# Kernel optimization log

Measured on AMD Instinct MI355X. Metric: run time of the kernel, lower is better.

The kernel has to match this reference:

```python
import math
import jax, jax.numpy as jnp
import numpy as np

B, N, W, D, H = 16, 64, 128, 128, 4

def posenc(L, d):
    pos = jnp.arange(L, dtype=jnp.float32)[:, None]
    div = jnp.exp(jnp.arange(0, d, 2, dtype=jnp.float32) * (-math.log(10000.0) / d))
    pe = jnp.zeros((L, d), jnp.float32)
    pe = pe.at[:, 0::2].set(jnp.sin(pos * div))
    pe = pe.at[:, 1::2].set(jnp.cos(pos * div))
    return pe

def ln(x):
    # torch nn.LayerNorm(x.shape[1:]) created fresh each call: normalize over all non-batch dims, no affine
    ax = tuple(range(1, x.ndim))
    m = x.mean(ax, keepdims=True)
    v = ((x - m) ** 2).mean(ax, keepdims=True)
    return (x - m) / jnp.sqrt(v + 1e-5)

def conv1d(x, w, b):
    # x [B,C,L], w [Cout,Cin,K] (torch layout), VALID padding
    y = jax.lax.conv_general_dilated(x, w, (1,), 'VALID', dimension_numbers=('NCH', 'OIH', 'NCH'))
    return y + b[None, :, None]

def convt1d(x, w, b, stride, pad):
    # torch ConvTranspose1d, w [Cin,Cout,K]
    K = w.shape[2]
    w_ = jnp.flip(w, 2).transpose(1, 0, 2)  # [Cout,Cin,K]
    y = jax.lax.conv_general_dilated(x, w_, (1,), [(K - 1 - pad, K - 1 - pad)],
                                     lhs_dilation=(stride,), dimension_numbers=('NCH', 'OIH', 'NCH'))
    return y + b[None, :, None]

def mha(q, k, v, wi, bi, wo, bo):
    # torch nn.MultiheadAttention(batch_first=True), H heads
    d = q.shape[-1]
    qp = q @ wi[:d].T + bi[:d]
    kp = k @ wi[d:2 * d].T + bi[d:2 * d]
    vp = v @ wi[2 * d:].T + bi[2 * d:]
    def heads(t):
        b_, l_, _ = t.shape
        return t.reshape(b_, l_, H, d // H).transpose(0, 2, 1, 3)
    qh, kh, vh = heads(qp), heads(kp), heads(vp)
    s = jnp.einsum('bhqd,bhkd->bhqk', qh, kh) / jnp.sqrt(jnp.asarray(d // H, qh.dtype))
    o = jnp.einsum('bhqk,bhkd->bhqd', jax.nn.softmax(s, -1), vh)
    b_, l_ = q.shape[0], q.shape[1]
    return o.transpose(0, 2, 1, 3).reshape(b_, l_, d) @ wo.T + bo


def setup_inputs():
    key = jax.random.key(0)
    ks = iter(jax.random.split(key, 64))
    def w(shape, s=0.05):
        return jax.random.normal(next(ks), shape, jnp.float32) * s
    inp = {}
    inp['tokens'] = jax.random.randint(next(ks), (B, N, W), 0, 257, jnp.int32)
    inp['emb_table'] = w((257, D), 1.0)
    for nm in ['ce', 'ct', 'cg', 'ces', 'cts']:
        inp['w_' + nm] = w((D, D, 3))
        inp['b_' + nm] = w((D,))
    inp['mha_wi'] = w((3 * D, D)); inp['mha_bi'] = w((3 * D,))
    inp['mha_wo'] = w((D, D)); inp['mha_bo'] = w((D,))
    s = 1.0 / math.sqrt(D)
    inp['tgt1'] = jax.random.uniform(next(ks), (1, D), jnp.float32, -s, s)
    inp['tgt2'] = jax.random.uniform(next(ks), (1, D), jnp.float32, -s, s)
    for nm in ['mu', 'lv', 'di']:
        inp['w_' + nm] = w((D, D)); inp['b_' + nm] = w((D,))
    inp['eps'] = jax.random.normal(next(ks), (B, D), jnp.float32)
    inp['dk_w'] = w((32, 32)); inp['dk_b'] = w((32,))
    inp['dv_w'] = w((32, 32)); inp['dv_b'] = w((32,))
    inp['wt1'] = w((32, 64, 3)); inp['bt1'] = w((64,))
    inp['wt2'] = w((64, 128, 3)); inp['bt2'] = w((128,))
    for nm in ['sq', 'sk', 'sv']:
        inp[nm + '_w'] = w((128, 128)); inp[nm + '_b'] = w((128,))
    inp['wt3'] = w((128, 128, 3)); inp['bt3'] = w((128,))
    return inp


def reference(tokens, emb_table, w_ce, b_ce, w_ct, b_ct, w_cg, b_cg, w_ces, b_ces, w_cts, b_cts,
              mha_wi, mha_bi, mha_wo, mha_bo, tgt1, tgt2,
              w_mu, b_mu, w_lv, b_lv, w_di, b_di, eps,
              dk_w, dk_b, dv_w, dv_b, wt1, bt1, wt2, bt2,
              sq_w, sq_b, sk_w, sk_b, sv_w, sv_b, wt3, bt3):
    emb = emb_table[tokens] + posenc(W, D)                    # [B,N,W,D]
    flat = emb.reshape(B * N, W, D)                           # batch the per-sample torch loop

    def word_branch(wc, bc, act):
        h = act(conv1d(flat.transpose(0, 2, 1), wc, bc)).transpose(0, 2, 1)  # [BN,W-2,D]
        return mha(h, h, h, mha_wi, mha_bi, mha_wo, mha_bo)

    a_e = jax.nn.elu(word_branch(w_ce, b_ce, jax.nn.elu))
    a_t = jnp.tanh(word_branch(w_ct, b_ct, jnp.tanh))
    xw = ln((a_e * a_t).reshape(B, N, W - 2, D)).reshape(B * N, W - 2, D)

    h = jax.nn.elu(conv1d(xw.transpose(0, 2, 1), w_cg, b_cg)).transpose(0, 2, 1)  # [BN,W-4,D]
    q1 = jnp.broadcast_to(tgt1[None], (B * N, 1, D))
    out = mha(q1, h, h, mha_wi, mha_bi, mha_wo, mha_bo)[:, 0, :].reshape(B, N, D)

    se = out + posenc(N, D)                                   # sentence level

    def sent_branch(wc, bc, act):
        hh = act(conv1d(se.transpose(0, 2, 1), wc, bc)).transpose(0, 2, 1)       # [B,N-2,D]
        return mha(hh, hh, hh, mha_wi, mha_bi, mha_wo, mha_bo)

    s_e = jax.nn.elu(sent_branch(w_ces, b_ces, jax.nn.elu))
    s_t = jnp.tanh(sent_branch(w_cts, b_cts, jnp.tanh))
    xs = ln(s_e * s_t)
    q2 = jnp.broadcast_to(tgt2[None], (B, 1, D))
    doc = mha(q2, xs, xs, mha_wi, mha_bi, mha_wo, mha_bo)[:, 0, :]

    mu = doc @ w_mu.T + b_mu
    lv = doc @ w_lv.T + b_lv
    z = mu + eps * jnp.exp(0.5 * lv)

    h = (z @ w_di.T + b_di).reshape(B, 32, -1)                # [B,32,4]
    L = h.shape[2]
    k = jnp.einsum('oi,bil->bol', dk_w, h) + dk_b[None, :, None]
    v = jnp.einsum('oi,bil->bol', dv_w, h) + dv_b[None, :, None]
    kh = k.reshape(B, H, 8, L)
    vh = v.reshape(B, H, 8, L)
    att = jax.nn.softmax(jnp.einsum('bhdl,bhdm->bhlm', kh, vh) / jnp.sqrt(8.0), -1)
    h = jax.nn.elu(jnp.einsum('bhlm,bhdm->bhld', att, vh).reshape(B, 32, L))
    h = jax.nn.elu(ln(convt1d(h, wt1, bt1, 2, 1)))            # [B,64,7]
    h = jax.nn.elu(ln(convt1d(h, wt2, bt2, 2, 1)))            # [B,128,13]
    L2 = h.shape[2]
    qc = jnp.einsum('oi,bil->bol', sq_w, h) + sq_b[None, :, None]
    kc = jnp.einsum('oi,bil->bol', sk_w, h) + sk_b[None, :, None]
    vc = jnp.einsum('oi,bil->bol', sv_w, h) + sv_b[None, :, None]
    qh = qc.reshape(B, H, 32, L2)
    khh = kc.reshape(B, H, 32, L2)
    att = jax.nn.softmax(jnp.einsum('bhdl,bhdm->bhlm', qh, khh) / jnp.sqrt(32.0), -1)
    vr = vc.reshape(B, H, 32, L2).reshape(B, H, L2, 32)       # faithful torch .view reinterpretation
    h = jax.nn.elu(jnp.einsum('bhlm,bhmd->bhld', att, vr).reshape(B, 128, L2))
    recon = jax.nn.sigmoid(ln(convt1d(h, wt3, bt3, 1, 1)))    # [B,128,13]
    return recon, mu, lv
```

## Files before the change

kernel.cpp:

```cpp
#include <hip/hip_runtime.h>
#include <hip/hip_bf16.h>

typedef __hip_bfloat16 bf16;
typedef __attribute__((ext_vector_type(8))) short bf16x8;
typedef __attribute__((ext_vector_type(4))) float f32x4;

__device__ __forceinline__ float b2f(bf16 x){ return __bfloat162float(x); }
__device__ __forceinline__ bf16  f2b(float x){ return __float2bfloat16(x); }
__device__ __forceinline__ unsigned short b2u(bf16 x){ union{bf16 b; unsigned short u;} c; c.b = x; return c.u; }

#define LOG2E 1.4426950408889634f
#define QSC (0.17677669529663687f * LOG2E)

__device__ __forceinline__ float fexp2(float x){
  float r; asm("v_exp_f32 %0, %1" : "=v"(r) : "v"(x)); return r;
}
__device__ __forceinline__ float fast_exp(float x){ return fexp2(x * LOG2E); }
__device__ __forceinline__ float eluf(float x){ return x > 0.f ? x : fast_exp(x) - 1.f; }
__device__ __forceinline__ float fast_tanh(float x){
  float cx = fminf(fmaxf(x, -15.f), 15.f);
  float t = fexp2(cx * (2.f*LOG2E));
  return (t - 1.f) / (t + 1.f);
}

#define PE_C (-0.07195578415606394f)

__device__ __forceinline__ float pe_val(int pos, int d){
  int j2 = d & ~1;
  float ang = (float)pos * expf((float)j2 * PE_C);
  return (d & 1) ? cosf(ang) : sinf(ang);
}

__device__ __forceinline__ void pack_one(const float* __restrict__ W, bf16* __restrict__ out,
                                         int K, int N, int conv, int qscale, int t){
  int j = t & 7, lane = (t >> 3) & 63;
  int rest = t >> 9; int NT = N >> 4;
  int nt = rest % NT; int kb = rest / NT;
  int k = kb*32 + ((lane >> 4) << 3) + j;
  int n = nt*16 + (lane & 15);
  float v = conv ? W[n*384 + (k & 127)*3 + (k >> 7)] : W[(long)n*K + k];
  if (qscale && n < 128) v *= QSC;
  out[t] = f2b(v);
}

__global__ void k_prep(const float* __restrict__ w_ce, const float* __restrict__ w_ct,
                       const float* __restrict__ w_cg, const float* __restrict__ w_ces,
                       const float* __restrict__ w_cts, const float* __restrict__ wi,
                       const float* __restrict__ wo,
                       bf16* P_CE, bf16* P_CT, bf16* P_CG, bf16* P_CES, bf16* P_CTS,
                       bf16* P_WI, bf16* P_WO, float* __restrict__ pet){
  int bid = blockIdx.x;
  if (bid < 1152){
    int grp = bid / 192; int t = (bid % 192)*256 + threadIdx.x;
    const float* W; bf16* out; int K, N, conv, qs = 0;
    if      (grp == 0){ W = w_ce;  out = P_CE;  K=384; N=128; conv=1; }
    else if (grp == 1){ W = w_ct;  out = P_CT;  K=384; N=128; conv=1; }
    else if (grp == 2){ W = w_cg;  out = P_CG;  K=384; N=128; conv=1; }
    else if (grp == 3){ W = w_ces; out = P_CES; K=384; N=128; conv=1; }
    else if (grp == 4){ W = w_cts; out = P_CTS; K=384; N=128; conv=1; }
    else              { W = wi;    out = P_WI;  K=128; N=384; conv=0; qs=1; }
    pack_one(W, out, K, N, conv, qs, t);
  } else if (bid < 1216){
    int t = (bid - 1152)*256 + threadIdx.x;
    pack_one(wo, P_WO, 128, 128, 0, 0, t);
  } else {
    int i = (bid - 1216)*256 + threadIdx.x;
    if (i < 16384) pet[i] = pe_val(i >> 7, i & 127);
  }
}

__global__ void k_qprep(const float* __restrict__ wi, const float* __restrict__ bi,
                        const float* __restrict__ t1, const float* __restrict__ t2,
                        float* __restrict__ rkv){
  int tid = threadIdx.x;
  __shared__ float qps[256];
  {
    int which = tid >> 7, jj = tid & 127;
    const float* t = which ? t2 : t1;
    float a = bi[jj];
    for (int i = 0; i < 128; ++i) a += wi[jj*128 + i] * t[i];
    qps[tid] = a;
  }
  __syncthreads();
  int i = tid & 127, which = tid >> 7;
  for (int h = 0; h < 4; ++h){
    float a = 0.f;
    for (int d = 0; d < 32; ++d) a += qps[which*128 + h*32 + d] * wi[(128 + h*32 + d)*128 + i];
    rkv[which*512 + h*128 + i] = a;
  }
}

__global__ void k_embed8(const int* __restrict__ tok, const float* __restrict__ tab,
                         const float* __restrict__ pet, bf16* __restrict__ out){
  int t = blockIdx.x*256 + threadIdx.x;
  int q = t & 15;
  int flat = t >> 4; int w = flat & 127;
  int tk = tok[flat];
  const float* ta = tab + tk*128 + q*8;
  const float* pe = pet + (w << 7) + q*8;
  bf16 ob[8];
  #pragma unroll
  for (int i = 0; i < 8; ++i) ob[i] = f2b(ta[i] + pe[i]);
  *(f32x4*)(out + (size_t)t*8) = *(f32x4*)ob;
}

__global__ void k_se(const bf16* __restrict__ in, const float* __restrict__ pet, bf16* __restrict__ out){
  int idx = blockIdx.x*256 + threadIdx.x;
  int d = idx & 127; int n = (idx >> 7) & 63;
  out[idx] = f2b(b2f(in[idx]) + pet[(n << 7) + d]);
}

__global__ __launch_bounds__(256)
void k_gemm_mfma(const bf16* __restrict__ A, const bf16* __restrict__ Bp_, const bf16* __restrict__ Bp2,
                 const float* __restrict__ bias_, const float* __restrict__ bias2,
                 bf16* __restrict__ C_, bf16* __restrict__ C2p,
                 const bf16* __restrict__ mul,
                 int M, int K, int a_lout, int a_lind, int lda,
                 int NT, int n0t, int ldc, int act_, int act2,
                 const float* __restrict__ lnst, int lngrp){
  const bf16* Bp = Bp_; const float* bias = bias_; bf16* C = C_; int act = act_;
  if (blockIdx.z){ Bp = Bp2; bias = bias2; C = C2p; act = act2; }

  __shared__ f32x4 AsV[2][512];
  char* As0 = (char*)AsV[0];
  char* As1 = (char*)AsV[1];
  int tid = threadIdx.x;
  int lane = tid & 63, wave = tid >> 6;
  int wm = wave >> 1, wn = wave & 1;
  int m0 = blockIdx.x*128;
  int by = blockIdx.y;

  long offA[2]; bool okA[2]; float lnm[2], lnr[2]; int sbyte[2];
  #pragma unroll
  for (int p = 0; p < 2; ++p){
    int e = tid + p*256;
    int row = e >> 2, kq = e & 3, m = m0 + row;
    okA[p] = (m < M);
    long off = 0;
    if (okA[p]){
      off = (a_lout > 0) ? (long)(m / a_lout)*a_lind + (long)(m % a_lout)*128 + kq*8
                         : (long)m*lda + kq*8;
    }
    offA[p] = off;
    lnm[p] = 0.f; lnr[p] = 1.f;
    if (lnst && okA[p]){ int g = (int)(off / (long)lngrp); lnm[p] = lnst[2*g]; lnr[p] = lnst[2*g+1]; }
    sbyte[p] = (row*64 + kq*16) ^ ((row & 7) << 4);
  }
  auto loadA = [&](int p, int kb)->float4{
    float4 v = make_float4(0.f,0.f,0.f,0.f);
    if (okA[p]){
      v = *(const float4*)(A + offA[p] + kb*32);
      if (lnst){
        bf16* pp = (bf16*)&v; bf16 oo[8];
        #pragma unroll
        for (int u = 0; u < 8; ++u) oo[u] = f2b((b2f(pp[u]) - lnm[p]) * lnr[p]);
        v = *(float4*)&oo[0];
      }
    }
    return v;
  };

  const bf16* bptr[4];
  size_t bstep = (size_t)NT*512;
  #pragma unroll
  for (int fn = 0; fn < 4; ++fn){
    int ntile = n0t + by*8 + wn*4 + fn;
    bptr[fn] = Bp + ((size_t)ntile*64 + lane)*8;
  }
  int abyte[4];
  #pragma unroll
  for (int fm = 0; fm < 4; ++fm){
    int row = wm*64 + fm*16 + (lane & 15);
    abyte[fm] = (row*64 + ((lane >> 4) << 4)) ^ ((row & 7) << 4);
  }

  f32x4 acc[4][4];
  #pragma unroll
  for (int i = 0; i < 4; ++i)
    #pragma unroll
    for (int j = 0; j < 4; ++j) acc[i][j] = (f32x4){0.f,0.f,0.f,0.f};

  float4 va0 = loadA(0, 0), va1 = loadA(1, 0);
  *(float4*)(As0 + sbyte[0]) = va0;
  *(float4*)(As0 + sbyte[1]) = va1;
  __syncthreads();

  int nk = K >> 5;
  for (int kb = 0; kb < nk; ++kb){
    char* cur = (kb & 1) ? As1 : As0;
    char* nxt = (kb & 1) ? As0 : As1;
    bool more = (kb + 1) < nk;
    if (more){ va0 = loadA(0, kb+1); va1 = loadA(1, kb+1); }
    bf16x8 bfr[4];
    #pragma unroll
    for (int fn = 0; fn < 4; ++fn) bfr[fn] = *(const bf16x8*)(bptr[fn] + (size_t)kb*bstep);
    bf16x8 afr[4];
    #pragma unroll
    for (int fm = 0; fm < 4; ++fm) afr[fm] = *(const bf16x8*)(cur + abyte[fm]);
    #pragma unroll
    for (int fm = 0; fm < 4; ++fm)
      #pragma unroll
      for (int fn = 0; fn < 4; ++fn)
        acc[fm][fn] = __builtin_amdgcn_mfma_f32_16x16x32_bf16(afr[fm], bfr[fn], acc[fm][fn], 0, 0, 0);
    if (more){
      *(float4*)(nxt + sbyte[0]) = va0;
      *(float4*)(nxt + sbyte[1]) = va1;
    }
    __syncthreads();
  }

  #pragma unroll
  for (int fm = 0; fm < 4; ++fm){
    #pragma unroll
    for (int r = 0; r < 4; ++r){
      int m = m0 + wm*64 + fm*16 + ((lane >> 4) << 2) + r;
      if (m >= M) continue;
      #pragma unroll
      for (int fn = 0; fn < 4; ++fn){
        int n = by*128 + wn*64 + fn*16 + (lane & 15);
        float v = acc[fm][fn][r] + (bias ? bias[n] : 0.f);
        if (act == 1) v = eluf(v);
        else if (act == 2) v = fast_tanh(v);
        if (mul) v *= b2f(mul[(long)m*ldc + n]);
        C[(long)m*ldc + n] = f2b(v);
      }
    }
  }
}

template<int L>
__global__ __launch_bounds__(256)
void k_attn_fused(const bf16* __restrict__ X, const bf16* __restrict__ Pwi,
                  const float* __restrict__ bi, bf16* __restrict__ o){
  constexpr int KB  = (L + 31) / 32;
  constexpr int MT  = KB * 2;
  constexpr int WMT = MT / 4;
  constexpr int NP  = KB * 32;
  constexpr int PRS = NP * 2;

  __shared__ alignas(16) char As[NP*256];
  __shared__ alignas(16) char Qb[NP*64];
  __shared__ alignas(16) char Kb[NP*64];
  __shared__ alignas(16) char Vt[32*PRS];
  char* Pb = As;

  int tid = threadIdx.x;
  int s = blockIdx.x >> 2, h = blockIdx.x & 3;
  const bf16* xb = X + (size_t)s*L*128;

  for (int e = tid; e < NP*16; e += 256){
    int row = e >> 4, c = e & 15;
    float4 v = make_float4(0.f,0.f,0.f,0.f);
    if (row < L) v = *(const float4*)(xb + (size_t)row*128 + c*8);
    *(float4*)(As + ((row*256 + c*16) ^ ((row & 7) << 4))) = v;
  }
  __syncthreads();

  int lane = tid & 63, wave = tid >> 6;
  int col = lane & 15;

  __builtin_amdgcn_s_setprio(1);
  #pragma unroll
  for (int mt = 0; mt < WMT; ++mt){
    int mtile = wave*WMT + mt;
    int arow = mtile*16 + col;
    bf16x8 a4[4];
    #pragma unroll
    for (int kb = 0; kb < 4; ++kb)
      a4[kb] = *(const bf16x8*)(As + ((arow*256 + kb*64 + ((lane >> 4) << 4)) ^ ((arow & 7) << 4)));
    #pragma unroll
    for (int which = 0; which < 3; ++which){
      f32x4 av[2];
      #pragma unroll
      for (int nt = 0; nt < 2; ++nt){
        int ntile = which*8 + h*2 + nt;
        float bia = bi[which*128 + h*32 + nt*16 + col];
        if (which == 0) bia *= QSC;
        av[nt] = (f32x4){bia, bia, bia, bia};
        #pragma unroll
        for (int kb = 0; kb < 4; ++kb){
          bf16x8 bfr = *(const bf16x8*)(Pwi + (((size_t)kb*24 + ntile)*64 + lane)*8);
          av[nt] = __builtin_amdgcn_mfma_f32_16x16x32_bf16(a4[kb], bfr, av[nt], 0, 0, 0);
        }
      }
      #pragma unroll
      for (int r = 0; r < 4; ++r){
        int row = mtile*16 + ((lane >> 4) << 2) + r;
        if (which < 2){
          unsigned pk = (unsigned)b2u(f2b(av[0][r])) | ((unsigned)b2u(f2b(av[1][r])) << 16);
          char* dst = which ? Kb : Qb;
          *(unsigned*)(dst + ((row*64 + col*4) ^ ((row & 7) << 4))) = pk;
        } else {
          int pos = (row & 15)*MT + (row >> 4);
          #pragma unroll
          for (int nt = 0; nt < 2; ++nt){
            int d = nt*16 + col;
            *(bf16*)(Vt + ((d*PRS + pos*2) ^ ((d & 7) << 4))) = f2b(av[nt][r]);
          }
        }
      }
    }
  }
  __builtin_amdgcn_s_setprio(0);
  __syncthreads();

  f32x4 acc[WMT][MT];
  #pragma unroll
  for (int mt = 0; mt < WMT; ++mt)
    #pragma unroll
    for (int nt = 0; nt < MT; ++nt) acc[mt][nt] = (f32x4){0.f,0.f,0.f,0.f};

  bf16x8 af[WMT];
  #pragma unroll
  for (int mt = 0; mt < WMT; ++mt){
    int row = (wave*WMT + mt)*16 + col;
    af[mt] = *(const bf16x8*)(Qb + ((row*64 + ((lane >> 4) << 4)) ^ ((row & 7) << 4)));
  }
  __builtin_amdgcn_s_setprio(1);
  #pragma unroll
  for (int nt = 0; nt < MT; ++nt){
    int rk2 = nt*16 + col;
    bf16x8 bfk = *(const bf16x8*)(Kb + ((rk2*64 + ((lane >> 4) << 4)) ^ ((rk2 & 7) << 4)));
    #pragma unroll
    for (int mt = 0; mt < WMT; ++mt)
      acc[mt][nt] = __builtin_amdgcn_mfma_f32_16x16x32_bf16(af[mt], bfk, acc[mt][nt], 0, 0, 0);
  }
  __builtin_amdgcn_s_setprio(0);

  const bool lastMask = col >= (L - (MT-1)*16);
  float pinv[WMT][4];
  #pragma unroll
  for (int mt = 0; mt < WMT; ++mt){
    #pragma unroll
    for (int r = 0; r < 4; ++r){
      float mx = -1e30f;
      #pragma unroll
      for (int nt = 0; nt < MT; ++nt){
        float v = acc[mt][nt][r];
        if (nt == MT-1 && lastMask){ v = -1e30f; acc[mt][nt][r] = v; }
        mx = fmaxf(mx, v);
      }
      mx = fmaxf(mx, __shfl_xor(mx, 1));
      mx = fmaxf(mx, __shfl_xor(mx, 2));
      mx = fmaxf(mx, __shfl_xor(mx, 4));
      mx = fmaxf(mx, __shfl_xor(mx, 8));
      float sum = 0.f;
      bf16 prow[MT];
      #pragma unroll
      for (int nt = 0; nt < MT; ++nt){
        float p = fexp2(acc[mt][nt][r] - mx);
        prow[nt] = f2b(p);
        sum += p;
      }
      sum += __shfl_xor(sum, 1);
      sum += __shfl_xor(sum, 2);
      sum += __shfl_xor(sum, 4);
      sum += __shfl_xor(sum, 8);
      pinv[mt][r] = 1.f / sum;
      int row = (wave*WMT + mt)*16 + ((lane >> 4) << 2) + r;
      char* dst = Pb + ((row*PRS + col*(MT*2)) ^ ((row & 7) << 4));
      if constexpr (MT == 8) *(f32x4*)dst = *(f32x4*)prow;
      else                   *(float2*)dst = *(float2*)prow;
    }
  }

  #pragma unroll
  for (int mt = 0; mt < WMT; ++mt){
    int mtile = wave*WMT + mt;
    f32x4 o0 = (f32x4){0.f,0.f,0.f,0.f}, o1 = (f32x4){0.f,0.f,0.f,0.f};
    __builtin_amdgcn_s_setprio(1);
    #pragma unroll
    for (int kb = 0; kb < KB; ++kb){
      int row = mtile*16 + col;
      bf16x8 pa = *(const bf16x8*)(Pb + ((row*PRS + kb*64 + ((lane >> 4) << 4)) ^ ((row & 7) << 4)));
      int d0 = col;
      bf16x8 v0 = *(const bf16x8*)(Vt + ((d0*PRS + kb*64 + ((lane >> 4) << 4)) ^ ((d0 & 7) << 4)));
      bf16x8 v1 = *(const bf16x8*)(Vt + (((d0+16)*PRS + kb*64 + ((lane >> 4) << 4)) ^ (((d0+16) & 7) << 4)));
      o0 = __builtin_amdgcn_mfma_f32_16x16x32_bf16(pa, v0, o0, 0, 0, 0);
      o1 = __builtin_amdgcn_mfma_f32_16x16x32_bf16(pa, v1, o1, 0, 0, 0);
    }
    __builtin_amdgcn_s_setprio(0);
    #pragma unroll
    for (int r = 0; r < 4; ++r){
      int row = mtile*16 + ((lane >> 4) << 2) + r;
      if (row < L){
        size_t ob = ((size_t)s*L + row)*128 + h*32 + col;
        o[ob]      = f2b(o0[r] * pinv[mt][r]);
        o[ob + 16] = f2b(o1[r] * pinv[mt][r]);
      }
    }
  }
}

template<int L>
__global__ __launch_bounds__(256)
void k_attn_tgt(const bf16* __restrict__ hin, const float* __restrict__ rk,
                const float* __restrict__ wi, const float* __restrict__ bi,
                bf16* __restrict__ outp){
  __shared__ alignas(16) char Hs[L*256];
  __shared__ float RKs[512];
  __shared__ float Ps[512];
  __shared__ float Cs[512];
  int tid = threadIdx.x, lane = tid & 63, wave = tid >> 6;
  int s = blockIdx.x;
  const bf16* hb = hin + (size_t)s*L*128;
  for (int e = tid; e < L*16; e += 256){
    int row = e >> 4, c = e & 15;
    *(float4*)(Hs + row*256 + ((c ^ (row & 7)) << 4)) = *(const float4*)(hb + row*128 + c*8);
  }
  for (int e = tid; e < 512; e += 256) RKs[e] = rk[e];
  __syncthreads();

  int j0 = lane, j1 = lane + 64;
  float v0 = -1e30f, v1 = -1e30f;
  if (j0 < L){
    float a = 0.f;
    #pragma unroll
    for (int c = 0; c < 16; ++c){
      bf16x8 x = *(const bf16x8*)(Hs + j0*256 + ((c ^ (j0 & 7)) << 4));
      #pragma unroll
      for (int u = 0; u < 8; ++u) a += b2f(((bf16*)&x)[u]) * RKs[wave*128 + c*8 + u];
    }
    v0 = a * 0.17677669529663687f;
  }
  if (j1 < L){
    float a = 0.f;
    #pragma unroll
    for (int c = 0; c < 16; ++c){
      bf16x8 x = *(const bf16x8*)(Hs + j1*256 + ((c ^ (j1 & 7)) << 4));
      #pragma unroll
      for (int u = 0; u < 8; ++u) a += b2f(((bf16*)&x)[u]) * RKs[wave*128 + c*8 + u];
    }
    v1 = a * 0.17677669529663687f;
  }
  float mx = fmaxf(v0, v1);
  #pragma unroll
  for (int off = 32; off; off >>= 1) mx = fmaxf(mx, __shfl_xor(mx, off));
  float e0 = (j0 < L) ? fast_exp(v0 - mx) : 0.f;
  float e1 = (j1 < L) ? fast_exp(v1 - mx) : 0.f;
  float sum = e0 + e1;
  #pragma unroll
// ... 285 lines not shown
  float a = bias[co];
  for (int k = 0; k < 3; ++k){
    int t = lo + pad - k;
    if (t < 0 || (t % stride)) continue;
    int li = t / stride;
    if (li >= Lin) continue;
    float aa = 0.f;
    for (int ci = 0; ci < Ci; ++ci) aa += xs[ci*Lin + li] * w[(size_t)ci*Co*3 + co*3 + k];
    a += aa;
  }
  y[(size_t)b*Co*Lout + co*Lout + lo] = a;
}

extern "C" void kernel_launch(void* const* d_in, const int* in_sizes, int n_in,
                              void* d_out, int out_size, void* d_ws, size_t ws_size,
                              hipStream_t stream){
  const int*   tokens = (const int*)  d_in[0];
  const float* tab    = (const float*)d_in[1];
  const float* w_ce = (const float*)d_in[2];  const float* b_ce = (const float*)d_in[3];
  const float* w_ct = (const float*)d_in[4];  const float* b_ct = (const float*)d_in[5];
  const float* w_cg = (const float*)d_in[6];  const float* b_cg = (const float*)d_in[7];
  const float* w_ces= (const float*)d_in[8];  const float* b_ces= (const float*)d_in[9];
  const float* w_cts= (const float*)d_in[10]; const float* b_cts= (const float*)d_in[11];
  const float* wi   = (const float*)d_in[12]; const float* bi   = (const float*)d_in[13];
  const float* wo   = (const float*)d_in[14]; const float* bo   = (const float*)d_in[15];
  const float* tgt1 = (const float*)d_in[16]; const float* tgt2 = (const float*)d_in[17];
  const float* w_mu = (const float*)d_in[18]; const float* b_mu = (const float*)d_in[19];
  const float* w_lv = (const float*)d_in[20]; const float* b_lv = (const float*)d_in[21];
  const float* w_di = (const float*)d_in[22]; const float* b_di = (const float*)d_in[23];
  const float* epsb = (const float*)d_in[24];
  const float* dk_w = (const float*)d_in[25]; const float* dk_b = (const float*)d_in[26];
  const float* dv_w = (const float*)d_in[27]; const float* dv_b = (const float*)d_in[28];
  const float* wt1  = (const float*)d_in[29]; const float* bt1  = (const float*)d_in[30];
  const float* wt2  = (const float*)d_in[31]; const float* bt2  = (const float*)d_in[32];
  const float* sq_w = (const float*)d_in[33]; const float* sq_b = (const float*)d_in[34];
  const float* sk_w = (const float*)d_in[35]; const float* sk_b = (const float*)d_in[36];
  const float* sv_w = (const float*)d_in[37]; const float* sv_b = (const float*)d_in[38];
  const float* wt3  = (const float*)d_in[39]; const float* bt3  = (const float*)d_in[40];

  float* dout = (float*)d_out;

  char* ws = (char*)d_ws;
  size_t off = 0;
  auto take = [&](size_t bytes)->char*{ char* p = ws + off; off += (bytes + 255) & ~(size_t)255; return p; };
  bf16* EMB  = (bf16*)take(16777216ull*2);
  bf16* HB   = (bf16*)take(16515072ull*2);
  bf16* OB   = (bf16*)take(16515072ull*2);
  bf16* AE   = (bf16*)take(16515072ull*2);
  bf16* O1   = (bf16*)take(131072ull*2);
  bf16* OUTB = (bf16*)take(131072ull*2);
  bf16* SEB  = (bf16*)take(131072ull*2);
  bf16* SH   = (bf16*)take(126976ull*2);
  bf16* SCT  = (bf16*)take(126976ull*2);
  bf16* SO   = (bf16*)take(126976ull*2);
  bf16* SAE  = (bf16*)take(126976ull*2);
  bf16* XS   = (bf16*)take(126976ull*2);
  bf16* DO1  = (bf16*)take(2048ull*2);
  bf16* DOC  = (bf16*)take(2048ull*2);
  float* RK  = (float*)take(1024*4);
  float* PART= (float*)take(2016ull*2*4);
  float* STATS=(float*)take(32*4);
  float* DEC2= (float*)take(7168*4);
  float* C2  = (float*)take(26624*4);
  float* DEC3= (float*)take(26624*4);
  float* QC  = (float*)take(26624*4);
  float* KC  = (float*)take(26624*4);
  float* VC  = (float*)take(26624*4);
  float* DEC4= (float*)take(26624*4);
  float* C3  = (float*)take(26624*4);
  float* PET = (float*)take(16384*4);
  bf16* P_CE = (bf16*)take(49152ull*2);
  bf16* P_CT = (bf16*)take(49152ull*2);
  bf16* P_CG = (bf16*)take(49152ull*2);
  bf16* P_CES= (bf16*)take(49152ull*2);
  bf16* P_CTS= (bf16*)take(49152ull*2);
  bf16* P_WI = (bf16*)take(49152ull*2);
  bf16* P_WO = (bf16*)take(16384ull*2);
  (void)ws_size; (void)in_sizes; (void)n_in; (void)out_size;

  auto cdiv = [](long a, long b){ return (int)((a + b - 1)/b); };
  auto gemm = [&](const bf16* A, const bf16* Bpp, const float* bias, bf16* C, const bf16* mul,
                  int M, int N, int K, int a_lout, int a_lind, int lda, int NT, int n0t, int ldc, int act,
                  const float* lnst, int lngrp){
    dim3 g(cdiv(M,128), N/128, 1);
    k_gemm_mfma<<<g, 256, 0, stream>>>(A, Bpp, Bpp, bias, bias, C, C, mul,
                                       M, K, a_lout, a_lind, lda, NT, n0t, ldc, act, act, lnst, lngrp);
  };
  auto gemmz = [&](const bf16* A, const bf16* Bp1, const float* b1, bf16* C1, int act1,
                   const bf16* Bp2, const float* b2, bf16* C2p, int act2,
                   int M, int N, int K, int a_lout, int a_lind, int lda, int NT, int n0t, int ldc){
    dim3 g(cdiv(M,128), N/128, 2);
    k_gemm_mfma<<<g, 256, 0, stream>>>(A, Bp1, Bp2, b1, b2, C1, C2p, nullptr,
                                       M, K, a_lout, a_lind, lda, NT, n0t, ldc, act1, act2, nullptr, 0);
  };

  k_prep<<<1280, 256, 0, stream>>>(w_ce, w_ct, w_cg, w_ces, w_cts, wi, wo,
                                   P_CE, P_CT, P_CG, P_CES, P_CTS, P_WI, P_WO, PET);
  k_qprep<<<1, 256, 0, stream>>>(wi, bi, tgt1, tgt2, RK);
  k_embed8<<<8192, 256, 0, stream>>>(tokens, tab, PET, EMB);

  gemmz(EMB, P_CE, b_ce, HB, 1, P_CT, b_ct, OB, 2, 129024, 128, 384, 126, 16384, 0, 8, 0, 128);

  k_attn_fused<126><<<4096, 256, 0, stream>>>(HB, P_WI, bi, EMB);
  gemm(EMB, P_WO, bo, AE, nullptr, 129024, 128, 128, 0, 0, 128, 8, 0, 128, 1, nullptr, 0);

  k_attn_fused<126><<<4096, 256, 0, stream>>>(OB, P_WI, bi, EMB);
  gemm(EMB, P_WO, bo, HB, AE, 129024, 128, 128, 0, 0, 128, 8, 0, 128, 2, nullptr, 0);

  k_ln_partial<<<2016, 256, 0, stream>>>(HB, PART, 1032192, 126);
  k_ln_fin<<<16, 256, 0, stream>>>(PART, STATS, 126, 1032192);

  gemm(HB, P_CG, b_cg, OB, nullptr, 126976, 128, 384, 124, 16128, 0, 8, 0, 128, 1, STATS, 1032192);

  k_attn_tgt<124><<<1024, 256, 0, stream>>>(OB, RK, wi, bi, O1);
  gemm(O1, P_WO, bo, OUTB, nullptr, 1024, 128, 128, 0, 0, 128, 8, 0, 128, 0, nullptr, 0);

  k_se<<<512, 256, 0, stream>>>(OUTB, PET, SEB);

  gemmz(SEB, P_CES, b_ces, SH, 1, P_CTS, b_cts, SCT, 2, 992, 128, 384, 62, 8192, 0, 8, 0, 128);

  k_attn_fused<62><<<64, 256, 0, stream>>>(SH, P_WI, bi, SO);
  gemm(SO, P_WO, bo, SAE, nullptr, 992, 128, 128, 0, 0, 128, 8, 0, 128, 1, nullptr, 0);

  k_attn_fused<62><<<64, 256, 0, stream>>>(SCT, P_WI, bi, SO);
  gemm(SO, P_WO, bo, SH, SAE, 992, 128, 128, 0, 0, 128, 8, 0, 128, 2, nullptr, 0);

  k_ln_small_bf16<<<16, 256, 0, stream>>>(SH, XS, 7936);

  k_attn_tgt<62><<<16, 256, 0, stream>>>(XS, RK + 512, wi, bi, DO1);
  gemm(DO1, P_WO, bo, DOC, nullptr, 16, 128, 128, 0, 0, 128, 8, 0, 128, 0, nullptr, 0);

  k_dec_a<<<16, 256, 0, stream>>>(DOC, w_mu, b_mu, w_lv, b_lv, epsb, w_di, b_di,
                                  dk_w, dk_b, dv_w, dv_b, wt1, bt1, dout, DEC2);
  k_convt<<<16*8, 256, 0, stream>>>(DEC2, wt2, bt2, C2, 16, 64, 128, 7, 13, 2, 1, 8);
  k_ln_small_f32<<<16, 256, 0, stream>>>(C2, DEC3, 1664, 1);
  k_chanproj3<<<cdiv(26624,256), 256, 0, stream>>>(DEC3, sq_w, sq_b, sk_w, sk_b, sv_w, sv_b,
                                                   QC, KC, VC, 16, 128, 13);
  k_dec_attn2<<<64, 256, 0, stream>>>(QC, KC, VC, DEC4);
  k_convt<<<16*8, 256, 0, stream>>>(DEC4, wt3, bt3, C3, 16, 128, 128, 13, 13, 1, 1, 8);
  k_ln_small_f32<<<16, 256, 0, stream>>>(C3, dout, 1664, 3);
}
```

Baseline: 656.5 us.

## Fuse all heads and the output projection into one attention kernel per sequence

Each attention block now processes one whole sequence and loops over all four heads in-block, instead of launching one block per head. The per-head outputs are kept in shared memory and fed straight into an in-kernel output projection with bias, activation and the optional multiply, which removes the separate GEMM launch and the global round-trip of the attention output. A second packed copy of the output weight is prepared with a permuted K order to match the shared-memory output layout. The cost is far fewer blocks (1024 instead of 4096, or 16 for the small stage), much larger shared memory per block (lower occupancy), and serialized heads inside each block.

```diff
diff --git a/kernel.cpp b/kernel.cpp
--- a/kernel.cpp
+++ b/kernel.cpp
@@ -32,13 +32,15 @@
 }
 
 __device__ __forceinline__ void pack_one(const float* __restrict__ W, bf16* __restrict__ out,
-                                         int K, int N, int conv, int qscale, int t){
+                                         int K, int N, int conv, int qscale, int kperm, int t){
   int j = t & 7, lane = (t >> 3) & 63;
   int rest = t >> 9; int NT = N >> 4;
   int nt = rest % NT; int kb = rest / NT;
   int k = kb*32 + ((lane >> 4) << 3) + j;
   int n = nt*16 + (lane & 15);
-  float v = conv ? W[n*384 + (k & 127)*3 + (k >> 7)] : W[(long)n*K + k];
+  int kt = k;
+  if (kperm){ int p = k & 31; kt = (k & ~31) | (((p & 1) << 4) | (p >> 1)); }
+  float v = conv ? W[n*384 + (kt & 127)*3 + (kt >> 7)] : W[(long)n*K + kt];
   if (qscale && n < 128) v *= QSC;
   out[t] = f2b(v);
 }
@@ -48,7 +50,7 @@
                        const float* __restrict__ w_cts, const float* __restrict__ wi,
                        const float* __restrict__ wo,
                        bf16* P_CE, bf16* P_CT, bf16* P_CG, bf16* P_CES, bf16* P_CTS,
-                       bf16* P_WI, bf16* P_WO, float* __restrict__ pet){
+                       bf16* P_WI, bf16* P_WO, bf16* P_WO2, float* __restrict__ pet){
   int bid = blockIdx.x;
   if (bid < 1152){
     int grp = bid / 192; int t = (bid % 192)*256 + threadIdx.x;
@@ -59,12 +61,15 @@
     else if (grp == 3){ W = w_ces; out = P_CES; K=384; N=128; conv=1; }
     else if (grp == 4){ W = w_cts; out = P_CTS; K=384; N=128; conv=1; }
     else              { W = wi;    out = P_WI;  K=128; N=384; conv=0; qs=1; }
-    pack_one(W, out, K, N, conv, qs, t);
+    pack_one(W, out, K, N, conv, qs, 0, t);
   } else if (bid < 1216){
     int t = (bid - 1152)*256 + threadIdx.x;
-    pack_one(wo, P_WO, 128, 128, 0, 0, t);
+    pack_one(wo, P_WO, 128, 128, 0, 0, 0, t);
+  } else if (bid < 1280){
+    int t = (bid - 1216)*256 + threadIdx.x;
+    pack_one(wo, P_WO2, 128, 128, 0, 0, 1, t);
   } else {
-    int i = (bid - 1216)*256 + threadIdx.x;
+    int i = (bid - 1280)*256 + threadIdx.x;
     if (i < 16384) pet[i] = pe_val(i >> 7, i & 127);
   }
 }
@@ -230,22 +235,24 @@
 
 template<int L>
 __global__ __launch_bounds__(256)
-void k_attn_fused(const bf16* __restrict__ X, const bf16* __restrict__ Pwi,
-                  const float* __restrict__ bi, bf16* __restrict__ o){
-  constexpr int KB  = (L + 31) / 32;
-  constexpr int MT  = KB * 2;
-  constexpr int WMT = MT / 4;
-  constexpr int NP  = KB * 32;
+void k_attn2(const bf16* __restrict__ X, const bf16* __restrict__ Pwi,
+             const float* __restrict__ bi, const bf16* __restrict__ Pwo2,
+             const float* __restrict__ bo, const bf16* __restrict__ mul,
+             bf16* __restrict__ out, int act){
+  constexpr int NP  = ((L + 31) / 32) * 32;
+  constexpr int RT  = NP / 16;
+  constexpr int WRT = RT / 4;
+  constexpr int KBP = NP / 32;
   constexpr int PRS = NP * 2;
 
   __shared__ alignas(16) char As[NP*256];
-  __shared__ alignas(16) char Qb[NP*64];
-  __shared__ alignas(16) char Kb[NP*64];
-  __shared__ alignas(16) char Vt[32*PRS];
+  __shared__ alignas(16) char QOb[NP*256];
+  __shared__ alignas(16) char Kb[NP*256];
+  __shared__ alignas(16) char Vt[128*NP*2];
   char* Pb = As;
 
   int tid = threadIdx.x;
-  int s = blockIdx.x >> 2, h = blockIdx.x & 3;
+  int s = blockIdx.x;
   const bf16* xb = X + (size_t)s*L*128;
 
   for (int e = tid; e < NP*16; e += 256){
@@ -261,15 +268,16 @@
 
   __builtin_amdgcn_s_setprio(1);
   #pragma unroll
-  for (int mt = 0; mt < WMT; ++mt){
-    int mtile = wave*WMT + mt;
+  for (int mt = 0; mt < WRT; ++mt){
+    int mtile = wave*WRT + mt;
     int arow = mtile*16 + col;
     bf16x8 a4[4];
     #pragma unroll
     for (int kb = 0; kb < 4; ++kb)
       a4[kb] = *(const bf16x8*)(As + ((arow*256 + kb*64 + ((lane >> 4) << 4)) ^ ((arow & 7) << 4)));
     #pragma unroll
-    for (int which = 0; which < 3; ++which){
+    for (int pair = 0; pair < 12; ++pair){
+      int which = pair >> 2, h = pair & 3;
       f32x4 av[2];
       #pragma unroll
       for (int nt = 0; nt < 2; ++nt){
@@ -288,14 +296,14 @@
         int row = mtile*16 + ((lane >> 4) << 2) + r;
         if (which < 2){
           unsigned pk = (unsigned)b2u(f2b(av[0][r])) | ((unsigned)b2u(f2b(av[1][r])) << 16);
-          char* dst = which ? Kb : Qb;
-          *(unsigned*)(dst + ((row*64 + col*4) ^ ((row & 7) << 4))) = pk;
+          char* dst = which ? Kb : QOb;
+          *(unsigned*)(dst + ((row*256 + h*64 + col*4) ^ ((row & 7) << 4))) = pk;
         } else {
-          int pos = (row & 15)*MT + (row >> 4);
+          int posj = (row & 15)*RT + (row >> 4);
           #pragma unroll
           for (int nt = 0; nt < 2; ++nt){
-            int d = nt*16 + col;
-            *(bf16*)(Vt + ((d*PRS + pos*2) ^ ((d & 7) << 4))) = f2b(av[nt][r]);
+            int d = h*32 + nt*16 + col;
+            *(bf16*)(Vt + ((d*PRS + posj*2) ^ ((d & 7) << 4))) = f2b(av[nt][r]);
           }
         }
       }
@@ -304,89 +312,125 @@
   __builtin_amdgcn_s_setprio(0);
   __syncthreads();
 
-  f32x4 acc[WMT][MT];
-  #pragma unroll
-  for (int mt = 0; mt < WMT; ++mt)
-    #pragma unroll
-    for (int nt = 0; nt < MT; ++nt) acc[mt][nt] = (f32x4){0.f,0.f,0.f,0.f};
-
-  bf16x8 af[WMT];
-  #pragma unroll
-  for (int mt = 0; mt < WMT; ++mt){
-    int row = (wave*WMT + mt)*16 + col;
-    af[mt] = *(const bf16x8*)(Qb + ((row*64 + ((lane >> 4) << 4)) ^ ((row & 7) << 4)));
-  }
-  __builtin_amdgcn_s_setprio(1);
-  #pragma unroll
-  for (int nt = 0; nt < MT; ++nt){
-    int rk2 = nt*16 + col;
-    bf16x8 bfk = *(const bf16x8*)(Kb + ((rk2*64 + ((lane >> 4) << 4)) ^ ((rk2 & 7) << 4)));
-    #pragma unroll
-    for (int mt = 0; mt < WMT; ++mt)
-      acc[mt][nt] = __builtin_amdgcn_mfma_f32_16x16x32_bf16(af[mt], bfk, acc[mt][nt], 0, 0, 0);
-  }
-  __builtin_amdgcn_s_setprio(0);
-
-  const bool lastMask = col >= (L - (MT-1)*16);
-  float pinv[WMT][4];
-  #pragma unroll
-  for (int mt = 0; mt < WMT; ++mt){
-    #pragma unroll
-    for (int r = 0; r < 4; ++r){
-      float mx = -1e30f;
-      #pragma unroll
-      for (int nt = 0; nt < MT; ++nt){
-        float v = acc[mt][nt][r];
-        if (nt == MT-1 && lastMask){ v = -1e30f; acc[mt][nt][r] = v; }
-        mx = fmaxf(mx, v);
+  const bool lastMask = col >= (L - (RT-1)*16);
+
+  for (int h = 0; h < 4; ++h){
+    f32x4 acc[WRT][RT];
+    #pragma unroll
+    for (int mt = 0; mt < WRT; ++mt)
+      #pragma unroll
+      for (int nt = 0; nt < RT; ++nt) acc[mt][nt] = (f32x4){0.f,0.f,0.f,0.f};
+
+    bf16x8 af[WRT];
+    #pragma unroll
+    for (int mt = 0; mt < WRT; ++mt){
+      int row = (wave*WRT + mt)*16 + col;
+      af[mt] = *(const bf16x8*)(QOb + ((row*256 + h*64 + ((lane >> 4) << 4)) ^ ((row & 7) << 4)));
+    }
+    __builtin_amdgcn_s_setprio(1);
+    #pragma unroll
+    for (int nt = 0; nt < RT; ++nt){
+      int rk2 = nt*16 + col;
+      bf16x8 bfk = *(const bf16x8*)(Kb + ((rk2*256 + h*64 + ((lane >> 4) << 4)) ^ ((rk2 & 7) << 4)));
+      #pragma unroll
+      for (int mt = 0; mt < WRT; ++mt)
+        acc[mt][nt] = __builtin_amdgcn_mfma_f32_16x16x32_bf16(af[mt], bfk, acc[mt][nt], 0, 0, 0);
+    }
+    __builtin_amdgcn_s_setprio(0);
+
+    float pinv[WRT][4];
+    #pragma unroll
+    for (int mt = 0; mt < WRT; ++mt){
+      #pragma unroll
+      for (int r = 0; r < 4; ++r){
+        float mx = -1e30f;
+        #pragma unroll
+        for (int nt = 0; nt < RT; ++nt){
+          float v = acc[mt][nt][r];
+          if (nt == RT-1 && lastMask){ v = -1e30f; acc[mt][nt][r] = v; }
+          mx = fmaxf(mx, v);
+        }
+        mx = fmaxf(mx, __shfl_xor(mx, 1));
+        mx = fmaxf(mx, __shfl_xor(mx, 2));
+        mx = fmaxf(mx, __shfl_xor(mx, 4));
+        mx = fmaxf(mx, __shfl_xor(mx, 8));
+        float sum = 0.f;
+        bf16 prow[RT];
+        #pragma unroll
+        for (int nt = 0; nt < RT; ++nt){
+          float p = fexp2(acc[mt][nt][r] - mx);
+          prow[nt] = f2b(p);
+          sum += p;
+        }
+        sum += __shfl_xor(sum, 1);
+        sum += __shfl_xor(sum, 2);
+        sum += __shfl_xor(sum, 4);
+        sum += __shfl_xor(sum, 8);
+        pinv[mt][r] = 1.f / sum;
+        int row = (wave*WRT + mt)*16 + ((lane >> 4) << 2) + r;
+        char* dst = Pb + ((row*PRS + col*(RT*2)) ^ ((row & 7) << 4));
+        if constexpr (RT == 8) *(f32x4*)dst = *(f32x4*)prow;
+        else                   *(float2*)dst = *(float2*)prow;
       }
-      mx = fmaxf(mx, __shfl_xor(mx, 1));
-      mx = fmaxf(mx, __shfl_xor(mx, 2));
-      mx = fmaxf(mx, __shfl_xor(mx, 4));
-      mx = fmaxf(mx, __shfl_xor(mx, 8));
-      float sum = 0.f;
-      bf16 prow[MT];
-      #pragma unroll
-      for (int nt = 0; nt < MT; ++nt){
-        float p = fexp2(acc[mt][nt][r] - mx);
-        prow[nt] = f2b(p);
-        sum += p;
+    }
+
+    #pragma unroll
+    for (int mt = 0; mt < WRT; ++mt){
+      int mtile = wave*WRT + mt;
+      f32x4 o0 = (f32x4){0.f,0.f,0.f,0.f}, o1 = (f32x4){0.f,0.f,0.f,0.f};
+      __builtin_amdgcn_s_setprio(1);
+      #pragma unroll
+      for (int kb = 0; kb < KBP; ++kb){
+        int row = mtile*16 + col;
+        bf16x8 pa = *(const bf16x8*)(Pb + ((row*PRS + kb*64 + ((lane >> 4) << 4)) ^ ((row & 7) << 4)));
+        int d0 = h*32 + col, d1 = d0 + 16;
+        bf16x8 v0 = *(const bf16x8*)(Vt + ((d0*PRS + kb*64 + ((lane >> 4) << 4)) ^ ((d0 & 7) << 4)));
+        bf16x8 v1 = *(const bf16x8*)(Vt + ((d1*PRS + kb*64 + ((lane >> 4) << 4)) ^ ((d1 & 7) << 4)));
+        o0 = __builtin_amdgcn_mfma_f32_16x16x32_bf16(pa, v0, o0, 0, 0, 0);
+        o1 = __builtin_amdgcn_mfma_f32_16x16x32_bf16(pa, v1, o1, 0, 0, 0);
       }
-      sum += __shfl_xor(sum, 1);
-      sum += __shfl_xor(sum, 2);
-      sum += __shfl_xor(sum, 4);
-      sum += __shfl_xor(sum, 8);
-      pinv[mt][r] = 1.f / sum;
-      int row = (wave*WMT + mt)*16 + ((lane >> 4) << 2) + r;
-      char* dst = Pb + ((row*PRS + col*(MT*2)) ^ ((row & 7) << 4));
-      if constexpr (MT == 8) *(f32x4*)dst = *(f32x4*)prow;
-      else                   *(float2*)dst = *(float2*)prow;
-    }
-  }
-
-  #pragma unroll
-  for (int mt = 0; mt < WMT; ++mt){
-    int mtile = wave*WMT + mt;
-    f32x4 o0 = (f32x4){0.f,0.f,0.f,0.f}, o1 = (f32x4){0.f,0.f,0.f,0.f};
-    __builtin_amdgcn_s_setprio(1);
-    #pragma unroll
-    for (int kb = 0; kb < KB; ++kb){
-      int row = mtile*16 + col;
-      bf16x8 pa = *(const bf16x8*)(Pb + ((row*PRS + kb*64 + ((lane >> 4) << 4)) ^ ((row & 7) << 4)));
-      int d0 = col;
-      bf16x8 v0 = *(const bf16x8*)(Vt + ((d0*PRS + kb*64 + ((lane >> 4) << 4)) ^ ((d0 & 7) << 4)));
-      bf16x8 v1 = *(const bf16x8*)(Vt + (((d0+16)*PRS + kb*64 + ((lane >> 4) << 4)) ^ (((d0+16) & 7) << 4)));
-      o0 = __builtin_amdgcn_mfma_f32_16x16x32_bf16(pa, v0, o0, 0, 0, 0);
-      o1 = __builtin_amdgcn_mfma_f32_16x16x32_bf16(pa, v1, o1, 0, 0, 0);
-    }
-    __builtin_amdgcn_s_setprio(0);
-    #pragma unroll
-    for (int r = 0; r < 4; ++r){
-      int row = mtile*16 + ((lane >> 4) << 2) + r;
-      if (row < L){
-        size_t ob = ((size_t)s*L + row)*128 + h*32 + col;
-        o[ob]      = f2b(o0[r] * pinv[mt][r]);
-        o[ob + 16] = f2b(o1[r] * pinv[mt][r]);
+      __builtin_amdgcn_s_setprio(0);
+      #pragma unroll
+      for (int r = 0; r < 4; ++r){
+        int row = mtile*16 + ((lane >> 4) << 2) + r;
+        unsigned pk = (unsigned)b2u(f2b(o0[r] * pinv[mt][r])) |
+                      ((unsigned)b2u(f2b(o1[r] * pinv[mt][r])) << 16);
+        *(unsigned*)(QOb + ((row*256 + h*64 + col*4) ^ ((row & 7) << 4))) = pk;
+      }
+    }
+  }
+
+  #pragma unroll
+  for (int mt = 0; mt < WRT; ++mt){
+    int mtile = wave*WRT + mt;
+    int arow = mtile*16 + col;
+    bf16x8 aw[4];
+    #pragma unroll
+    for (int kb = 0; kb < 4; ++kb)
+      aw[kb] = *(const bf16x8*)(QOb + ((arow*256 + kb*64 + ((lane >> 4) << 4)) ^ ((arow & 7) << 4)));
+    #pragma unroll
+    for (int fn = 0; fn < 8; ++fn){
+      float bia = bo[fn*16 + col];
+      f32x4 wacc = (f32x4){bia, bia, bia, bia};
+      __builtin_amdgcn_s_setprio(1);
+      #pragma unroll
+      for (int kb = 0; kb < 4; ++kb){
+        bf16x8 bfr = *(const bf16x8*)(Pwo2 + (((size_t)kb*8 + fn)*64 + lane)*8);
+        wacc = __builtin_amdgcn_mfma_f32_16x16x32_bf16(aw[kb], bfr, wacc, 0, 0, 0);
+      }
+      __builtin_amdgcn_s_setprio(0);
+      #pragma unroll
+      for (int r = 0; r < 4; ++r){
+        int row = mtile*16 + ((lane >> 4) << 2) + r;
+        if (row < L){
+          int n = fn*16 + col;
+          float v = wacc[r];
+          if (act == 1) v = eluf(v);
+          else if (act == 2) v = fast_tanh(v);
+          size_t om = ((size_t)s*L + row)*128 + n;
+          if (mul) v *= b2f(mul[om]);
+          out[om] = f2b(v);
+        }
       }
     }
   }
@@ -778,7 +822,6 @@
   bf16* SEB  = (bf16*)take(131072ull*2);
   bf16* SH   = (bf16*)take(126976ull*2);
   bf16* SCT  = (bf16*)take(126976ull*2);
-  bf16* SO   = (bf16*)take(126976ull*2);
   bf16* SAE  = (bf16*)take(126976ull*2);
   bf16* XS   = (bf16*)take(126976ull*2);
   bf16* DO1  = (bf16*)take(2048ull*2);
@@ -802,6 +845,7 @@
   bf16* P_CTS= (bf16*)take(49152ull*2);
   bf16* P_WI = (bf16*)take(49152ull*2);
   bf16* P_WO = (bf16*)take(16384ull*2);
+  bf16* P_WO2= (bf16*)take(16384ull*2);
   (void)ws_size; (void)in_sizes; (void)n_in; (void)out_size;
 
   auto cdiv = [](long a, long b){ return (int)((a + b - 1)/b); };
@@ -820,18 +864,15 @@
                                        M, K, a_lout, a_lind, lda, NT, n0t, ldc, act1, act2, nullptr, 0);
   };
 
-  k_prep<<<1280, 256, 0, stream>>>(w_ce, w_ct, w_cg, w_ces, w_cts, wi, wo,
-                                   P_CE, P_CT, P_CG, P_CES, P_CTS, P_WI, P_WO, PET);
+  k_prep<<<1344, 256, 0, stream>>>(w_ce, w_ct, w_cg, w_ces, w_cts, wi, wo,
+                                   P_CE, P_CT, P_CG, P_CES, P_CTS, P_WI, P_WO, P_WO2, PET);
   k_qprep<<<1, 256, 0, stream>>>(wi, bi, tgt1, tgt2, RK);
   k_embed8<<<8192, 256, 0, stream>>>(tokens, tab, PET, EMB);
 
   gemmz(EMB, P_CE, b_ce, HB, 1, P_CT, b_ct, OB, 2, 129024, 128, 384, 126, 16384, 0, 8, 0, 128);
 
-  k_attn_fused<126><<<4096, 256, 0, stream>>>(HB, P_WI, bi, EMB);
-  gemm(EMB, P_WO, bo, AE, nullptr, 129024, 128, 128, 0, 0, 128, 8, 0, 128, 1, nullptr, 0);
-
-  k_attn_fused<126><<<4096, 256, 0, stream>>>(OB, P_WI, bi, EMB);
-  gemm(EMB, P_WO, bo, HB, AE, 129024, 128, 128, 0, 0, 128, 8, 0, 128, 2, nullptr, 0);
+  k_attn2<126><<<1024, 256, 0, stream>>>(HB, P_WI, bi, P_WO2, bo, nullptr, AE, 1);
+  k_attn2<126><<<1024, 256, 0, stream>>>(OB, P_WI, bi, P_WO2, bo, AE, HB, 2);
 
   k_ln_partial<<<2016, 256, 0, stream>>>(HB, PART, 1032192, 126);
   k_ln_fin<<<16, 256, 0, stream>>>(PART, STATS, 126, 1032192);
@@ -845,11 +886,8 @@
 
   gemmz(SEB, P_CES, b_ces, SH, 1, P_CTS, b_cts, SCT, 2, 992, 128, 384, 62, 8192, 0, 8, 0, 128);
 
-  k_attn_fused<62><<<64, 256, 0, stream>>>(SH, P_WI, bi, SO);
-  gemm(SO, P_WO, bo, SAE, nullptr, 992, 128, 128, 0, 0, 128, 8, 0, 128, 1, nullptr, 0);
-
-  k_attn_fused<62><<<64, 256, 0, stream>>>(SCT, P_WI, bi, SO);
-  gemm(SO, P_WO, bo, SH, SAE, 992, 128, 128, 0, 0, 128, 8, 0, 128, 2, nullptr, 0);
+  k_attn2<62><<<16, 256, 0, stream>>>(SH, P_WI, bi, P_WO2, bo, nullptr, SAE, 1);
+  k_attn2<62><<<16, 256, 0, stream>>>(SCT, P_WI, bi, P_WO2, bo, SAE, SH, 2);
 
   k_ln_small_bf16<<<16, 256, 0, stream>>>(SH, XS, 7936);
 
```

Result: slower. 703.2 us (+7.1%).

## Use direct global-to-LDS loads for GEMM A tiles and attention input staging

Applied to the files above, without the earlier changes.

Replaces the register round-trip (global load into VGPRs, then ds_write) with global_load_lds 16-byte DMA for the GEMM A operand and the fused attention input tile. The per-thread row/column mapping is permuted so the fixed per-wave contiguous LDS destination matches the existing XOR swizzle. This frees VGPRs and removes LDS write instructions. The GEMM path that applies LayerNorm on load keeps the old path, since DMA cannot transform data.

```diff
diff --git a/kernel.cpp b/kernel.cpp
--- a/kernel.cpp
+++ b/kernel.cpp
@@ -11,6 +11,10 @@
 
 #define LOG2E 1.4426950408889634f
 #define QSC (0.17677669529663687f * LOG2E)
+
+#define GLD16(gp, lp) __builtin_amdgcn_global_load_lds( \
+    (const __attribute__((address_space(1))) void*)(gp), \
+    (__attribute__((address_space(3))) void*)(lp), 16, 0, 0)
 
 __device__ __forceinline__ float fexp2(float x){
   float r; asm("v_exp_f32 %0, %1" : "=v"(r) : "v"(x)); return r;
@@ -110,6 +114,7 @@
   out[idx] = f2b(b2f(in[idx]) + pet[(n << 7) + d]);
 }
 
+template<bool GLL>
 __global__ __launch_bounds__(256)
 void k_gemm_mfma(const bf16* __restrict__ A, const bf16* __restrict__ Bp_, const bf16* __restrict__ Bp2,
                  const float* __restrict__ bias_, const float* __restrict__ bias2,
@@ -134,7 +139,15 @@
   #pragma unroll
   for (int p = 0; p < 2; ++p){
     int e = tid + p*256;
-    int row = e >> 2, kq = e & 3, m = m0 + row;
+    int row, kq;
+    if (GLL){
+      int x = e;
+      row = (((x >> 3) << 1) | (((x >> 2) ^ (x >> 4)) & 1)) & 127;
+      kq  = ((((x >> 1) ^ (x >> 3)) & 1) << 1) | ((x ^ (x >> 2) ^ (x >> 4)) & 1);
+    } else {
+      row = e >> 2; kq = e & 3;
+    }
+    int m = m0 + row;
     okA[p] = (m < M);
     long off = 0;
     if (okA[p]){
@@ -143,22 +156,9 @@
     }
     offA[p] = off;
     lnm[p] = 0.f; lnr[p] = 1.f;
-    if (lnst && okA[p]){ int g = (int)(off / (long)lngrp); lnm[p] = lnst[2*g]; lnr[p] = lnst[2*g+1]; }
+    if (!GLL && lnst && okA[p]){ int g = (int)(off / (long)lngrp); lnm[p] = lnst[2*g]; lnr[p] = lnst[2*g+1]; }
     sbyte[p] = (row*64 + kq*16) ^ ((row & 7) << 4);
   }
-  auto loadA = [&](int p, int kb)->float4{
-    float4 v = make_float4(0.f,0.f,0.f,0.f);
-    if (okA[p]){
-      v = *(const float4*)(A + offA[p] + kb*32);
-      if (lnst){
-        bf16* pp = (bf16*)&v; bf16 oo[8];
-        #pragma unroll
-        for (int u = 0; u < 8; ++u) oo[u] = f2b((b2f(pp[u]) - lnm[p]) * lnr[p]);
-        v = *(float4*)&oo[0];
-      }
-    }
-    return v;
-  };
 
   const bf16* bptr[4];
   size_t bstep = (size_t)NT*512;
@@ -180,33 +180,76 @@
     #pragma unroll
     for (int j = 0; j < 4; ++j) acc[i][j] = (f32x4){0.f,0.f,0.f,0.f};
 
-  float4 va0 = loadA(0, 0), va1 = loadA(1, 0);
-  *(float4*)(As0 + sbyte[0]) = va0;
-  *(float4*)(As0 + sbyte[1]) = va1;
-  __syncthreads();
-
   int nk = K >> 5;
-  for (int kb = 0; kb < nk; ++kb){
-    char* cur = (kb & 1) ? As1 : As0;
-    char* nxt = (kb & 1) ? As0 : As1;
-    bool more = (kb + 1) < nk;
-    if (more){ va0 = loadA(0, kb+1); va1 = loadA(1, kb+1); }
-    bf16x8 bfr[4];
-    #pragma unroll
-    for (int fn = 0; fn < 4; ++fn) bfr[fn] = *(const bf16x8*)(bptr[fn] + (size_t)kb*bstep);
-    bf16x8 afr[4];
-    #pragma unroll
-    for (int fm = 0; fm < 4; ++fm) afr[fm] = *(const bf16x8*)(cur + abyte[fm]);
-    #pragma unroll
-    for (int fm = 0; fm < 4; ++fm)
-      #pragma unroll
-      for (int fn = 0; fn < 4; ++fn)
-        acc[fm][fn] = __builtin_amdgcn_mfma_f32_16x16x32_bf16(afr[fm], bfr[fn], acc[fm][fn], 0, 0, 0);
-    if (more){
-      *(float4*)(nxt + sbyte[0]) = va0;
-      *(float4*)(nxt + sbyte[1]) = va1;
-    }
+
+  if constexpr (GLL){
+    int ldsw = (tid >> 6)*1024;
+    #pragma unroll
+    for (int p = 0; p < 2; ++p)
+      GLD16(A + offA[p], As0 + p*4096 + ldsw);
     __syncthreads();
+    for (int kb = 0; kb < nk; ++kb){
+      char* cur = (kb & 1) ? As1 : As0;
+      char* nxt = (kb & 1) ? As0 : As1;
+      bool more = (kb + 1) < nk;
+      if (more){
+        #pragma unroll
+        for (int p = 0; p < 2; ++p)
+          GLD16(A + offA[p] + (kb+1)*32, nxt + p*4096 + ldsw);
+      }
+      bf16x8 bfr[4];
+      #pragma unroll
+      for (int fn = 0; fn < 4; ++fn) bfr[fn] = *(const bf16x8*)(bptr[fn] + (size_t)kb*bstep);
+      bf16x8 afr[4];
+      #pragma unroll
+      for (int fm = 0; fm < 4; ++fm) afr[fm] = *(const bf16x8*)(cur + abyte[fm]);
+      #pragma unroll
+      for (int fm = 0; fm < 4; ++fm)
+        #pragma unroll
+        for (int fn = 0; fn < 4; ++fn)
+          acc[fm][fn] = __builtin_amdgcn_mfma_f32_16x16x32_bf16(afr[fm], bfr[fn], acc[fm][fn], 0, 0, 0);
+      __syncthreads();
+    }
+  } else {
+    auto loadA = [&](int p, int kb)->float4{
+      float4 v = make_float4(0.f,0.f,0.f,0.f);
+      if (okA[p]){
+        v = *(const float4*)(A + offA[p] + kb*32);
+        if (lnst){
+          bf16* pp = (bf16*)&v; bf16 oo[8];
+          #pragma unroll
+          for (int u = 0; u < 8; ++u) oo[u] = f2b((b2f(pp[u]) - lnm[p]) * lnr[p]);
+          v = *(float4*)&oo[0];
+        }
+      }
+      return v;
+    };
+    float4 va0 = loadA(0, 0), va1 = loadA(1, 0);
+    *(float4*)(As0 + sbyte[0]) = va0;
+    *(float4*)(As0 + sbyte[1]) = va1;
+    __syncthreads();
+    for (int kb = 0; kb < nk; ++kb){
+      char* cur = (kb & 1) ? As1 : As0;
+      char* nxt = (kb & 1) ? As0 : As1;
+      bool more = (kb + 1) < nk;
+      if (more){ va0 = loadA(0, kb+1); va1 = loadA(1, kb+1); }
+      bf16x8 bfr[4];
+      #pragma unroll
+      for (int fn = 0; fn < 4; ++fn) bfr[fn] = *(const bf16x8*)(bptr[fn] + (size_t)kb*bstep);
+      bf16x8 afr[4];
+      #pragma unroll
+      for (int fm = 0; fm < 4; ++fm) afr[fm] = *(const bf16x8*)(cur + abyte[fm]);
+      #pragma unroll
+      for (int fm = 0; fm < 4; ++fm)
+        #pragma unroll
+        for (int fn = 0; fn < 4; ++fn)
+          acc[fm][fn] = __builtin_amdgcn_mfma_f32_16x16x32_bf16(afr[fm], bfr[fn], acc[fm][fn], 0, 0, 0);
+      if (more){
+        *(float4*)(nxt + sbyte[0]) = va0;
+        *(float4*)(nxt + sbyte[1]) = va1;
+      }
+      __syncthreads();
+    }
   }
 
   #pragma unroll
@@ -248,11 +291,17 @@
   int s = blockIdx.x >> 2, h = blockIdx.x & 3;
   const bf16* xb = X + (size_t)s*L*128;
 
-  for (int e = tid; e < NP*16; e += 256){
-    int row = e >> 4, c = e & 15;
-    float4 v = make_float4(0.f,0.f,0.f,0.f);
-    if (row < L) v = *(const float4*)(xb + (size_t)row*128 + c*8);
-    *(float4*)(As + ((row*256 + c*16) ^ ((row & 7) << 4))) = v;
+  {
+    constexpr int NCH = (NP*16)/256;
+    int ldsw = (tid >> 6)*1024;
+    #pragma unroll
+    for (int p = 0; p < NCH; ++p){
+      int x = p*256 + tid;
+      int row = x >> 4;
+      int c = (x & 15) ^ (row & 7);
+      const bf16* gp = (row < L) ? (xb + (size_t)row*128 + c*8) : xb;
+      GLD16(gp, As + p*4096 + ldsw);
+    }
   }
   __syncthreads();
 
@@ -809,15 +858,19 @@
                   int M, int N, int K, int a_lout, int a_lind, int lda, int NT, int n0t, int ldc, int act,
                   const float* lnst, int lngrp){
     dim3 g(cdiv(M,128), N/128, 1);
-    k_gemm_mfma<<<g, 256, 0, stream>>>(A, Bpp, Bpp, bias, bias, C, C, mul,
-                                       M, K, a_lout, a_lind, lda, NT, n0t, ldc, act, act, lnst, lngrp);
+    if (lnst)
+      k_gemm_mfma<false><<<g, 256, 0, stream>>>(A, Bpp, Bpp, bias, bias, C, C, mul,
+                                                M, K, a_lout, a_lind, lda, NT, n0t, ldc, act, act, lnst, lngrp);
+    else
+      k_gemm_mfma<true><<<g, 256, 0, stream>>>(A, Bpp, Bpp, bias, bias, C, C, mul,
+                                               M, K, a_lout, a_lind, lda, NT, n0t, ldc, act, act, nullptr, 0);
   };
   auto gemmz = [&](const bf16* A, const bf16* Bp1, const float* b1, bf16* C1, int act1,
                    const bf16* Bp2, const float* b2, bf16* C2p, int act2,
                    int M, int N, int K, int a_lout, int a_lind, int lda, int NT, int n0t, int ldc){
     dim3 g(cdiv(M,128), N/128, 2);
-    k_gemm_mfma<<<g, 256, 0, stream>>>(A, Bp1, Bp2, b1, b2, C1, C2p, nullptr,
-                                       M, K, a_lout, a_lind, lda, NT, n0t, ldc, act1, act2, nullptr, 0);
+    k_gemm_mfma<true><<<g, 256, 0, stream>>>(A, Bp1, Bp2, b1, b2, C1, C2p, nullptr,
+                                             M, K, a_lout, a_lind, lda, NT, n0t, ldc, act1, act2, nullptr, 0);
   };
 
   k_prep<<<1280, 256, 0, stream>>>(w_ce, w_ct, w_cg, w_ces, w_cts, wi, wo,
```

After: 629.5 us, median of 2. 1.04x faster.
